# Kernel optimization log

Hardware: AMD Instinct MI355X
Metric: run time of the kernel (lower is better)

Reference implementation:

```python
import jax, jax.numpy as jnp
import numpy as np

BATCH = 262144
NUM_CLASSES = 1000
K = 0.5
T = 3.0
ALPHA = 1.0
GAMMA = 2.0
# error_weights dict: {(i, (i+1) % NUM_CLASSES): 2.0 for i in range(100)}
ERROR_WEIGHTS = {(i, (i + 1) % NUM_CLASSES): 2.0 for i in range(100)}


def setup_inputs() -> dict:
    key = jax.random.key(0)
    k1, k2 = jax.random.split(key)
    output = jax.random.normal(k1, (BATCH, NUM_CLASSES), dtype=jnp.float32)
    target = jax.random.randint(k2, (BATCH,), 0, NUM_CLASSES)
    wt = np.zeros((NUM_CLASSES, NUM_CLASSES), dtype=np.float32)
    mk = np.zeros((NUM_CLASSES, NUM_CLASSES), dtype=bool)
    for (t_, p_), w in ERROR_WEIGHTS.items():
        wt[t_, p_] = w
        mk[t_, p_] = True
    return {
        "output": output,
        "target": target,
        "weight_table": jnp.asarray(wt),
        "in_dict": jnp.asarray(mk),
    }


def reference(output, target, weight_table, in_dict):
    b = output.shape[0]
    # per-sample cross entropy (stable log-softmax)
    logp = jax.nn.log_softmax(output, axis=-1)                     # [B, C]
    ce = -jnp.take_along_axis(logp, target[:, None], axis=1)[:, 0]  # [B]
    pt = jnp.exp(-ce)
    f_loss = ALPHA * (1.0 - pt) ** GAMMA * ce                      # [B]
    pred = jnp.argmax(output, axis=-1)                             # [B]
    # dense-table lookup replacing the per-sample Python dict loop
    w = weight_table[target, pred]                                 # [B]
    m = in_dict[target, pred]                                      # [B] bool
    loss1 = jnp.sum(jnp.where(m, f_loss * w, 0.0))
    loss2 = jnp.sum(jnp.where(m, 0.0, f_loss))
    l1 = loss1 / b
    l2 = loss2 / b
    w2 = jax.nn.sigmoid(K * (jax.lax.stop_gradient(l1) - T))
    total = jnp.where(loss1 > 0, l1 + w2 * l2, loss2 / b)
    return total
```

## Files before the change

### kernel.cpp

```cpp
#include <hip/hip_runtime.h>
#include <math.h>

#define BATCH 262144
#define NUM_CLASSES 1000
#define NF4 250

__global__ __launch_bounds__(256, 4) void dbfl_main(
    const float* __restrict__ output,
    const int* __restrict__ target,
    const float* __restrict__ wt,
    double* __restrict__ acc)
{
    const int lane = threadIdx.x & 63;
    const int wib  = threadIdx.x >> 6;
    const int wpb  = blockDim.x >> 6;
    const long long gwave  = (long long)blockIdx.x * wpb + wib;
    const long long nwaves = (long long)gridDim.x * wpb;

    float acc1 = 0.f, acc2 = 0.f;

    long long row = gwave;
    if (row < BATCH) {
        const float4* rp4 = (const float4*)(output + row * (long long)NUM_CLASSES);
        float4 vc[4];
#pragma unroll
        for (int c = 0; c < 4; ++c) {
            const int f = lane + 64 * c;
            vc[c] = (f < NF4) ? rp4[f]
                              : make_float4(-INFINITY, -INFINITY, -INFINITY, -INFINITY);
        }
        int tcur = target[row];

        for (;;) {
            const long long nrow = row + nwaves;
            const bool have_next = (nrow < BATCH);
            float4 vn[4];
            int tnext = 0;
            if (have_next) {
                const float4* np4 = (const float4*)(output + nrow * (long long)NUM_CLASSES);
#pragma unroll
                for (int c = 0; c < 4; ++c) {
                    const int f = lane + 64 * c;
                    vn[c] = (f < NF4) ? np4[f]
                                      : make_float4(-INFINITY, -INFINITY, -INFINITY, -INFINITY);
                }
                tnext = target[nrow];
            }

            float bm = -INFINITY;
#pragma unroll
            for (int c = 0; c < 4; ++c)
                bm = fmaxf(bm, fmaxf(fmaxf(vc[c].x, vc[c].y), fmaxf(vc[c].z, vc[c].w)));
            float wm = bm;
#pragma unroll
            for (int off = 32; off > 0; off >>= 1)
                wm = fmaxf(wm, __shfl_xor(wm, off, 64));

            int bi = 0x7fffffff;
#pragma unroll
            for (int c = 3; c >= 0; --c) {
                const int base = (lane + 64 * c) * 4;
                if (vc[c].w == wm) bi = base + 3;
                if (vc[c].z == wm) bi = base + 2;
                if (vc[c].y == wm) bi = base + 1;
                if (vc[c].x == wm) bi = base + 0;
            }
            int wi = bi;
#pragma unroll
            for (int off = 32; off > 0; off >>= 1)
                wi = min(wi, __shfl_xor(wi, off, 64));

            const int t_s  = __builtin_amdgcn_readfirstlane(tcur);
            const int wi_s = __builtin_amdgcn_readfirstlane(wi);
            const float w = wt[(long long)t_s * NUM_CLASSES + wi_s];

            float s = 0.f;
#pragma unroll
            for (int c = 0; c < 4; ++c) {
                s += __expf(vc[c].x - wm);
                s += __expf(vc[c].y - wm);
                s += __expf(vc[c].z - wm);
                s += __expf(vc[c].w - wm);
            }
#pragma unroll
            for (int off = 32; off > 0; off >>= 1)
                s += __shfl_xor(s, off, 64);

            const int f4  = t_s >> 2;
            const int src = f4 & 63;
            const int ch  = f4 >> 6;
            const int cm  = t_s & 3;
            float4 vsel = vc[0];
            if (ch == 1) vsel = vc[1];
            else if (ch == 2) vsel = vc[2];
            else if (ch == 3) vsel = vc[3];
            float cand = vsel.x;
            if (cm == 1) cand = vsel.y;
            else if (cm == 2) cand = vsel.z;
            else if (cm == 3) cand = vsel.w;
            const float xt = __shfl(cand, src, 64);

            const float ce = wm + __logf(s) - xt;
            const float pt = __expf(-ce);
            const float om_pt = 1.f - pt;
            const float fl = om_pt * om_pt * ce;
            if (lane == 0) {
                if (w != 0.f) acc1 += fl * w;
                else          acc2 += fl;
            }

            if (!have_next) break;
#pragma unroll
            for (int c = 0; c < 4; ++c) vc[c] = vn[c];
            tcur = tnext;
            row  = nrow;
        }
    }

    __shared__ float sh1[8], sh2[8];
    if (lane == 0) { sh1[wib] = acc1; sh2[wib] = acc2; }
    __syncthreads();
    if (threadIdx.x == 0) {
        float a = 0.f, b = 0.f;
        for (int i = 0; i < wpb; ++i) { a += sh1[i]; b += sh2[i]; }
        unsafeAtomicAdd(&acc[0], (double)a);
        unsafeAtomicAdd(&acc[1], (double)b);
    }
}

__global__ void dbfl_final(const double* __restrict__ acc, float* __restrict__ out)
{
    const double loss1 = acc[0];
    const double loss2 = acc[1];
    const double b  = (double)BATCH;
    const double l1 = loss1 / b;
    const double l2 = loss2 / b;
    const double w2 = 1.0 / (1.0 + exp(-0.5 * (l1 - 3.0)));
    const double total = (loss1 > 0.0) ? (l1 + w2 * l2) : l2;
    out[0] = (float)total;
}

extern "C" void kernel_launch(void* const* d_in, const int* in_sizes, int n_in,
                              void* d_out, int out_size, void* d_ws, size_t ws_size,
                              hipStream_t stream)
{
    const float* output = (const float*)d_in[0];
    const int*   target = (const int*)d_in[1];
    const float* wt     = (const float*)d_in[2];

    double* acc = (double*)d_ws;
    hipMemsetAsync(d_ws, 0, 2 * sizeof(double), stream);

    const int block = 256;
    const int grid  = 512;
    dbfl_main<<<grid, block, 0, stream>>>(output, target, wt, acc);
    dbfl_final<<<1, 1, 0, stream>>>(acc, (float*)d_out);
}
```

Measured before the change: 1.326 ms.

## Drop software prefetch, use nontemporal loads, raise occupancy and grid size

Removes the register double-buffered prefetch of the next row and processes one row per iteration in a plain grid-stride loop. Row loads become nontemporal, and occupancy is raised through the launch bound and an eightfold larger grid. Latency hiding now comes from having more resident waves instead of explicit prefetch, with the added cost of more blocks issuing atomics at the end.

```diff
diff --git a/kernel.cpp b/kernel.cpp
--- a/kernel.cpp
+++ b/kernel.cpp
@@ -5,7 +5,9 @@
 #define NUM_CLASSES 1000
 #define NF4 250
 
-__global__ __launch_bounds__(256, 4) void dbfl_main(
+typedef float f32x4 __attribute__((ext_vector_type(4)));
+
+__global__ __launch_bounds__(256, 6) void dbfl_main(
     const float* __restrict__ output,
     const int* __restrict__ target,
     const float* __restrict__ wt,
@@ -18,102 +20,79 @@
     const long long nwaves = (long long)gridDim.x * wpb;
 
     float acc1 = 0.f, acc2 = 0.f;
+    const f32x4 vpad = {-INFINITY, -INFINITY, -INFINITY, -INFINITY};
 
-    long long row = gwave;
-    if (row < BATCH) {
-        const float4* rp4 = (const float4*)(output + row * (long long)NUM_CLASSES);
-        float4 vc[4];
+    for (long long row = gwave; row < BATCH; row += nwaves) {
+        const f32x4* rp4 = (const f32x4*)(output + row * (long long)NUM_CLASSES);
+        const int tcur = target[row];
+
+        f32x4 vc[4];
 #pragma unroll
         for (int c = 0; c < 4; ++c) {
             const int f = lane + 64 * c;
-            vc[c] = (f < NF4) ? rp4[f]
-                              : make_float4(-INFINITY, -INFINITY, -INFINITY, -INFINITY);
+            vc[c] = (f < NF4) ? __builtin_nontemporal_load(rp4 + f) : vpad;
         }
-        int tcur = target[row];
 
-        for (;;) {
-            const long long nrow = row + nwaves;
-            const bool have_next = (nrow < BATCH);
-            float4 vn[4];
-            int tnext = 0;
-            if (have_next) {
-                const float4* np4 = (const float4*)(output + nrow * (long long)NUM_CLASSES);
+        float bm = -INFINITY;
 #pragma unroll
-                for (int c = 0; c < 4; ++c) {
-                    const int f = lane + 64 * c;
-                    vn[c] = (f < NF4) ? np4[f]
-                                      : make_float4(-INFINITY, -INFINITY, -INFINITY, -INFINITY);
-                }
-                tnext = target[nrow];
-            }
+        for (int c = 0; c < 4; ++c)
+            bm = fmaxf(bm, fmaxf(fmaxf(vc[c].x, vc[c].y), fmaxf(vc[c].z, vc[c].w)));
+        float wm = bm;
+#pragma unroll
+        for (int off = 32; off > 0; off >>= 1)
+            wm = fmaxf(wm, __shfl_xor(wm, off, 64));
 
-            float bm = -INFINITY;
+        int bi = 0x7fffffff;
 #pragma unroll
-            for (int c = 0; c < 4; ++c)
-                bm = fmaxf(bm, fmaxf(fmaxf(vc[c].x, vc[c].y), fmaxf(vc[c].z, vc[c].w)));
-            float wm = bm;
+        for (int c = 3; c >= 0; --c) {
+            const int base = (lane + 64 * c) * 4;
+            if (vc[c].w == wm) bi = base + 3;
+            if (vc[c].z == wm) bi = base + 2;
+            if (vc[c].y == wm) bi = base + 1;
+            if (vc[c].x == wm) bi = base + 0;
+        }
+        int wi = bi;
 #pragma unroll
-            for (int off = 32; off > 0; off >>= 1)
-                wm = fmaxf(wm, __shfl_xor(wm, off, 64));
+        for (int off = 32; off > 0; off >>= 1)
+            wi = min(wi, __shfl_xor(wi, off, 64));
 
-            int bi = 0x7fffffff;
+        const int t_s  = __builtin_amdgcn_readfirstlane(tcur);
+        const int wi_s = __builtin_amdgcn_readfirstlane(wi);
+        const float w = wt[(long long)t_s * NUM_CLASSES + wi_s];
+
+        float s = 0.f;
 #pragma unroll
-            for (int c = 3; c >= 0; --c) {
-                const int base = (lane + 64 * c) * 4;
-                if (vc[c].w == wm) bi = base + 3;
-                if (vc[c].z == wm) bi = base + 2;
-                if (vc[c].y == wm) bi = base + 1;
-                if (vc[c].x == wm) bi = base + 0;
-            }
-            int wi = bi;
+        for (int c = 0; c < 4; ++c) {
+            s += __expf(vc[c].x - wm);
+            s += __expf(vc[c].y - wm);
+            s += __expf(vc[c].z - wm);
+            s += __expf(vc[c].w - wm);
+        }
 #pragma unroll
-            for (int off = 32; off > 0; off >>= 1)
-                wi = min(wi, __shfl_xor(wi, off, 64));
+        for (int off = 32; off > 0; off >>= 1)
+            s += __shfl_xor(s, off, 64);
 
-            const int t_s  = __builtin_amdgcn_readfirstlane(tcur);
-            const int wi_s = __builtin_amdgcn_readfirstlane(wi);
-            const float w = wt[(long long)t_s * NUM_CLASSES + wi_s];
+        const int f4  = t_s >> 2;
+        const int src = f4 & 63;
+        const int ch  = f4 >> 6;
+        const int cm  = t_s & 3;
+        f32x4 vsel = vc[0];
+        if (ch == 1) vsel = vc[1];
+        else if (ch == 2) vsel = vc[2];
+        else if (ch == 3) vsel = vc[3];
+        float cand = vsel.x;
+        if (cm == 1) cand = vsel.y;
+        else if (cm == 2) cand = vsel.z;
+        else if (cm == 3) cand = vsel.w;
+        const float xt = __shfl(cand, src, 64);
 
-            float s = 0.f;
-#pragma unroll
-            for (int c = 0; c < 4; ++c) {
-                s += __expf(vc[c].x - wm);
-                s += __expf(vc[c].y - wm);
-                s += __expf(vc[c].z - wm);
-                s += __expf(vc[c].w - wm);
-            }
-#pragma unroll
-            for (int off = 32; off > 0; off >>= 1)
-                s += __shfl_xor(s, off, 64);
-
-            const int f4  = t_s >> 2;
-            const int src = f4 & 63;
-            const int ch  = f4 >> 6;
-            const int cm  = t_s & 3;
-            float4 vsel = vc[0];
-            if (ch == 1) vsel = vc[1];
-            else if (ch == 2) vsel = vc[2];
-            else if (ch == 3) vsel = vc[3];
-            float cand = vsel.x;
-            if (cm == 1) cand = vsel.y;
-            else if (cm == 2) cand = vsel.z;
-            else if (cm == 3) cand = vsel.w;
-            const float xt = __shfl(cand, src, 64);
-
-            const float ce = wm + __logf(s) - xt;
-            const float pt = __expf(-ce);
-            const float om_pt = 1.f - pt;
-            const float fl = om_pt * om_pt * ce;
-            if (lane == 0) {
-                if (w != 0.f) acc1 += fl * w;
-                else          acc2 += fl;
-            }
-
-            if (!have_next) break;
-#pragma unroll
-            for (int c = 0; c < 4; ++c) vc[c] = vn[c];
-            tcur = tnext;
-            row  = nrow;
+        const float ce = wm + __logf(s) - xt;
+        const float pt = __expf(-ce);
+        const float om_pt = 1.f - pt;
+        const float fl = om_pt * om_pt * ce;
+        if (lane == 0) {
+            if (w != 0.f) acc1 += fl * w;
+            else          acc2 += fl;
         }
     }
 
@@ -152,7 +131,7 @@
     hipMemsetAsync(d_ws, 0, 2 * sizeof(double), stream);
 
     const int block = 256;
-    const int grid  = 512;
+    const int grid  = 4096;
     dbfl_main<<<grid, block, 0, stream>>>(output, target, wt, acc);
     dbfl_final<<<1, 1, 0, stream>>>(acc, (float*)d_out);
 }
```

After: 1.294 ms. 2.4% less time.
